# Kernel tuning notes

Hardware: AMD Instinct MI355X
Metric: run time of the kernel (lower is better)

The kernel has to match this reference:

```python
import jax, jax.numpy as jnp
import numpy as np

B, T, C, NH, RD = 128, 512, 384, 6, 16
HD = C // NH
SEQ_LEN = 512


def setup_inputs() -> dict:
    key = jax.random.key(0)
    kx, kqkv, kout = jax.random.split(key, 3)
    x = jax.random.normal(kx, (B, T, C), dtype=jnp.float32)
    # torch nn.Linear weights are [out_features, in_features]
    Wqkv = jax.random.normal(kqkv, (3 * C, C), dtype=jnp.float32) * 0.02
    Wout = jax.random.normal(kout, (C, C), dtype=jnp.float32) * 0.02
    freqs = 1.0 / (10000.0 ** (jnp.arange(0, RD, 2, dtype=jnp.float32) / RD))  # [RD//2]
    f = jnp.outer(jnp.arange(SEQ_LEN, dtype=jnp.float32), freqs)  # [SEQ_LEN, RD//2]
    cos = jnp.cos(f)[None, None]  # [1,1,SEQ_LEN,RD//2]
    sin = jnp.sin(f)[None, None]
    return {"x": x, "Wqkv": Wqkv, "Wout": Wout, "cos": cos, "sin": sin}


def _rope(t, c, s, rd):
    # t: [B, NH, T, HD]; partial rotary on first rd channels
    r, p = t[..., :rd], t[..., rd:]
    r1, r2 = r[..., : rd // 2], r[..., rd // 2:]
    rot = jnp.concatenate([r1 * c - r2 * s, r2 * c + r1 * s], axis=-1)
    return jnp.concatenate([rot, p], axis=-1)


def reference(x, Wqkv, Wout, cos, sin):
    b, t, c = x.shape
    nh, hd, rd = NH, c // NH, RD
    qkv = jnp.einsum("btc,dc->btd", x, Wqkv).reshape(b, t, 3, nh, hd)
    q, k, v = (jnp.transpose(qkv[:, :, i], (0, 2, 1, 3)) for i in range(3))  # [b,nh,t,hd]
    cc = cos[:, :, :t]
    ss = sin[:, :, :t]
    q = _rope(q, cc, ss, rd)
    k = _rope(k, cc, ss, rd)
    scale = 1.0 / jnp.sqrt(jnp.asarray(hd, dtype=x.dtype))
    scores = jnp.einsum("bhqd,bhkd->bhqk", q, k) * scale
    causal = jnp.tril(jnp.ones((t, t), dtype=bool))
    scores = jnp.where(causal, scores, jnp.finfo(scores.dtype).min)
    att = jax.nn.softmax(scores, axis=-1)
    o = jnp.einsum("bhqk,bhkd->bhqd", att, v)  # [b,nh,t,hd]
    o = jnp.transpose(o, (0, 2, 1, 3)).reshape(b, t, c)
    return jnp.einsum("btc,dc->btd", o, Wout)
```

## Files before the change

kernel.cpp:

```cpp
#include <hip/hip_runtime.h>

#define B_DIM 128
#define T_DIM 512
#define C_DIM 384
#define NH_DIM 6
#define HD_DIM 64
#define QKV_LD 1152

typedef __bf16 bf16x8 __attribute__((ext_vector_type(8)));
typedef __bf16 bf16x4 __attribute__((ext_vector_type(4)));
typedef float f32x4 __attribute__((ext_vector_type(4)));

#define K_SCALE 0.18033688011112042f

__device__ __forceinline__ void gload_lds16(const __bf16* g, __bf16* l) {
  __builtin_amdgcn_global_load_lds(
      (const __attribute__((address_space(1))) void*)g,
      (__attribute__((address_space(3))) void*)l, 16, 0, 0);
}

#define X_F4 6291456
#define WQKV_F4 110592
#define WOUT_F4 36864
__global__ __launch_bounds__(256) void cast_all(const float* __restrict__ x,
                                                const float* __restrict__ wqkv,
                                                const float* __restrict__ wout,
                                                __bf16* __restrict__ xb,
                                                __bf16* __restrict__ wqkvb,
                                                __bf16* __restrict__ woutb) {
  int i = blockIdx.x * blockDim.x + threadIdx.x;
  const float4* src;
  bf16x4* dst;
  if (i < X_F4) {
    src = (const float4*)x + i;
    dst = (bf16x4*)xb + i;
  } else if (i < X_F4 + WQKV_F4) {
    src = (const float4*)wqkv + (i - X_F4);
    dst = (bf16x4*)wqkvb + (i - X_F4);
  } else {
    src = (const float4*)wout + (i - X_F4 - WQKV_F4);
    dst = (bf16x4*)woutb + (i - X_F4 - WQKV_F4);
  }
  float4 v = *src;
  bf16x4 o;
  o[0] = (__bf16)v.x; o[1] = (__bf16)v.y; o[2] = (__bf16)v.z; o[3] = (__bf16)v.w;
  *dst = o;
}

__global__ __launch_bounds__(256) void gemm_bt(const __bf16* __restrict__ A,
                                               const __bf16* __restrict__ Bm,
                                               __bf16* __restrict__ Cbq,
                                               __bf16* __restrict__ Cbk,
                                               __bf16* __restrict__ vt,
                                               float* __restrict__ Cf,
                                               const float* __restrict__ cosp,
                                               const float* __restrict__ sinp,
                                               int M, int N, int K) {
  __shared__ __attribute__((aligned(16))) __bf16 As[128 * 32];
  __shared__ __attribute__((aligned(16))) __bf16 Bs[128 * 32];
  const int nwg = gridDim.x * gridDim.y;
  const int bid = blockIdx.x + gridDim.x * blockIdx.y;
  const int per = nwg >> 3;
  const int swz = (bid & 7) * per + (bid >> 3);
  const int m0 = (swz / gridDim.x) * 128;
  const int n0 = (swz % gridDim.x) * 128;
  const int tid = threadIdx.x;
  const int wave = tid >> 6;
  const int lane = tid & 63;
  const int lr = lane & 15;
  const int quad = lane >> 4;
  const int wm = (wave & 1) * 64;
  const int wn = (wave >> 1) * 64;
  const int ca0 = wave * 2, ca1 = wave * 2 + 1;
  const int srow = lane >> 2;
  const int row0 = ca0 * 16 + srow, row1 = ca1 * 16 + srow;
  const int slot = (lane & 3) ^ ((lane >> 3) & 3);
  const int rs = (quad ^ ((lr >> 1) & 3)) * 8;
  const __bf16* pA0 = &A[(size_t)(m0 + row0) * K + slot * 8];
  const __bf16* pA1 = &A[(size_t)(m0 + row1) * K + slot * 8];
  const __bf16* pB0 = &Bm[(size_t)(n0 + row0) * K + slot * 8];
  const __bf16* pB1 = &Bm[(size_t)(n0 + row1) * K + slot * 8];
  f32x4 acc[4][4] = {};
  for (int k0 = 0; k0 < K; k0 += 32) {
    __syncthreads();
    gload_lds16(pA0, &As[ca0 * 512]);
    gload_lds16(pA1, &As[ca1 * 512]);
    gload_lds16(pB0, &Bs[ca0 * 512]);
    gload_lds16(pB1, &Bs[ca1 * 512]);
    pA0 += 32; pA1 += 32; pB0 += 32; pB1 += 32;
    __syncthreads();
    bf16x8 af[4], bf[4];
#pragma unroll
    for (int i = 0; i < 4; ++i)
      af[i] = *(bf16x8*)&As[(wm + i * 16 + lr) * 32 + rs];
#pragma unroll
    for (int j = 0; j < 4; ++j)
      bf[j] = *(bf16x8*)&Bs[(wn + j * 16 + lr) * 32 + rs];
#pragma unroll
    for (int i = 0; i < 4; ++i)
#pragma unroll
      for (int j = 0; j < 4; ++j)
        acc[i][j] = __builtin_amdgcn_mfma_f32_16x16x32_bf16(af[i], bf[j], acc[i][j], 0, 0, 0);
  }
  if (Cf) {
#pragma unroll
    for (int i = 0; i < 4; ++i)
#pragma unroll
      for (int j = 0; j < 4; ++j) {
        int gm = m0 + wm + i * 16 + quad * 4;
        int gn = n0 + wn + j * 16 + lr;
#pragma unroll
        for (int r = 0; r < 4; ++r) Cf[(size_t)(gm + r) * N + gn] = acc[i][j][r];
      }
    return;
  }
  if (n0 >= 2 * C_DIM) {
    const int tbase = (m0 & (T_DIM - 1)) + wm;
    const int bb = m0 >> 9;
    const int dcolbase = n0 - 2 * C_DIM + wn;
    const int tslotx = (lane & 7) ^ (lane >> 3);
#pragma unroll
    for (int pass = 0; pass < 2; ++pass) {
      __syncthreads();
      if ((wave >> 1) == pass) {
        __bf16* T = (wave & 1) ? Bs : As;
#pragma unroll
        for (int i = 0; i < 4; ++i)
#pragma unroll
          for (int j = 0; j < 4; ++j) {
            const int d = j * 16 + lr;
            const int sl = (i * 2 + (quad >> 1)) ^ (d & 7);
            bf16x4 w;
#pragma unroll
            for (int r = 0; r < 4; ++r) w[r] = (__bf16)acc[i][j][r];
            *(bf16x4*)&T[d * 64 + sl * 8 + (quad & 1) * 4] = w;
          }
#pragma unroll
        for (int it = 0; it < 8; ++it) {
          const int dl = it * 8 + (lane >> 3);
          bf16x8 v = *(bf16x8*)&T[dl * 64 + (lane & 7) * 8];
          const int dfull = dcolbase + dl;
          const int hh = dfull >> 6, dd = dfull & 63;
          *(bf16x8*)&vt[((size_t)(bb * NH_DIM + hh) * 64 + dd) * T_DIM + tbase +
                        tslotx * 8] = v;
        }
      }
    }
    return;
  }
  const bool isQ = (n0 < C_DIM);
  __bf16* dst = isQ ? Cbq : Cbk;
  const int colbase = n0 - (isQ ? 0 : C_DIM);
  const float qs = isQ ? K_SCALE : 1.0f;
#pragma unroll
  for (int i = 0; i < 4; ++i) {
#pragma unroll
    for (int j = 0; j < 4; ++j) {
      int gm = m0 + wm + i * 16 + quad * 4;
      int gn = colbase + wn + j * 16 + lr;
      const int cbase = colbase + wn + j * 16;
      const bool ropeBlk = ((cbase & 63) == 0);
      if (ropeBlk) {
#pragma unroll
        for (int r = 0; r < 4; ++r) {
          float v = acc[i][j][r];
          float p = __shfl_xor(v, 8, 64);
          int t = (gm + r) & (T_DIM - 1);
          float c = cosp[t * 8 + (lr & 7)];
          float s = sinp[t * 8 + (lr & 7)];
          v = (lr & 8) ? __builtin_fmaf(v, c, p * s)
                       : __builtin_fmaf(v, c, -p * s);
          dst[(size_t)(gm + r) * C_DIM + gn] = (__bf16)(v * qs);
        }
      } else {
#pragma unroll
        for (int r = 0; r < 4; ++r)
          dst[(size_t)(gm + r) * C_DIM + gn] = (__bf16)(acc[i][j][r] * qs);
      }
    }
  }
}

__global__ __launch_bounds__(256) void attn_kernel(const __bf16* __restrict__ qb,
                                                   const __bf16* __restrict__ kb,
                                                   const __bf16* __restrict__ vt,
                                                   __bf16* __restrict__ o) {
  __shared__ __attribute__((aligned(16))) __bf16 K0s[64 * 64];
  __shared__ __attribute__((aligned(16))) __bf16 K1s[64 * 64];
  __shared__ __attribute__((aligned(16))) __bf16 V0s[64 * 64];
  __shared__ __attribute__((aligned(16))) __bf16 V1s[64 * 64];
  const int bid = blockIdx.x;
  const int swz = (bid & 7) * 384 + (bid >> 3);
  const int pair = swz & 3;
  const int h = (swz >> 2) % NH_DIM;
  const int b = swz / (4 * NH_DIM);
  const int qlo = pair, qhi = 7 - pair;
  const int tid = threadIdx.x;
  const int wave = tid >> 6;
  const int lane = tid & 63;
  const int lr = lane & 15;
  const int quad = lane >> 4;
  const __bf16* qbase = qb + (size_t)b * T_DIM * C_DIM + h * HD_DIM;
  const __bf16* kbase = kb + (size_t)b * T_DIM * C_DIM + h * HD_DIM;
  const __bf16* vtb = vt + (size_t)(b * NH_DIM + h) * HD_DIM * T_DIM;
  const int qrow_lo = qlo * 64 + wave * 16;
  const int qrow_hi = qhi * 64 + wave * 16;
  bf16x8 qfl[2], qfh[2];
#pragma unroll
  for (int ks = 0; ks < 2; ++ks) {
    qfl[ks] = *(const bf16x8*)&qbase[(size_t)(qrow_lo + lr) * C_DIM + ks * 32 + quad * 8];
    qfh[ks] = *(const bf16x8*)&qbase[(size_t)(qrow_hi + lr) * C_DIM + ks * 32 + quad * 8];
  }
  f32x4 oaL[4] = {}, oaH[4] = {};
  f32x4 lL = {}, lH = {};
  bf16x8 vones;
#pragma unroll
  for (int e = 0; e < 8; ++e) vones[e] = (__bf16)1.0f;
  const int skey = (((lane >> 3) & 3) << 1) | (wave & 1);
  const int gsl = ((lane & 7) ^ skey) * 8;
  const int grA = wave * 8 + (lane >> 3);
  const int grB = grA + 32;
  const int ldsA = wave * 512;
  const int ldsB = (wave + 4) * 512;
  auto stage = [&](int kt, __bf16* KT, __bf16* VT) {
    const __bf16* ks = kbase + (size_t)(kt * 64) * C_DIM;
    const __bf16* vs = vtb + kt * 64;
    gload_lds16(&ks[(size_t)grA * C_DIM + gsl], KT + ldsA);
    gload_lds16(&ks[(size_t)grB * C_DIM + gsl], KT + ldsB);
    gload_lds16(&vs[(size_t)grA * T_DIM + gsl], VT + ldsA);
    gload_lds16(&vs[(size_t)grB * T_DIM + gsl], VT + ldsB);
  };
  const int keyK = ((lr & 3) << 1) | ((lr >> 2) & 1);
  const int keyV = ((lr & 3) << 1) | ((lr >> 3) & 1);
  const int swK0 = (quad ^ keyK) * 8, swK1 = ((4 + quad) ^ keyK) * 8;
  const int swV0 = (quad ^ keyV) * 8, swV1 = ((4 + quad) ^ keyV) * 8;
  const int rkbase = ((lr >> 2) & 3) * 8 + (lr & 3);
  auto body = [&](const __bf16* KT, const __bf16* VT, const bf16x8 (&qf)[2],
                  f32x4 (&oa)[4], f32x4& lacc, int myq, bool diag, int kt) {
    f32x4 sj[4];
#pragma unroll
    for (int j = 0; j < 4; ++j) {
      const int rK = (j >> 1) * 32 + (j & 1) * 4 + rkbase;
      bf16x8 kf0 = *(const bf16x8*)&KT[rK * 64 + swK0];
      bf16x8 kf1 = *(const bf16x8*)&KT[rK * 64 + swK1];
      f32x4 z = {};
      z = __builtin_amdgcn_mfma_f32_16x16x32_bf16(kf0, qf[0], z, 0, 0, 0);
      z = __builtin_amdgcn_mfma_f32_16x16x32_bf16(kf1, qf[1], z, 0, 0, 0);
      sj[j] = z;
    }
    if (diag) {
#pragma unroll
      for (int j = 0; j < 4; ++j)
#pragma unroll
        for (int r = 0; r < 4; ++r) {
          int key = kt * 64 + (j >> 1) * 32 + quad * 8 + (j & 1) * 4 + r;
          if (key > myq) sj[j][r] = -3.0e38f;
        }
    }
    bf16x8 pf0, pf1;
#pragma unroll
    for (int j = 0; j < 4; ++j)
#pragma unroll
      for (int r = 0; r < 4; ++r) {
        float pv = exp2f(sj[j][r]);
        const int jj = (j & 1) * 4 + r;
        if (j < 2) pf0[jj] = (__bf16)pv; else pf1[jj] = (__bf16)pv;
      }
#pragma unroll
    for (int dt = 0; dt < 4; ++dt) {
      bf16x8 vf0 = *(const bf16x8*)&VT[(dt * 16 + lr) * 64 + swV0];
      bf16x8 vf1 = *(const bf16x8*)&VT[(dt * 16 + lr) * 64 + swV1];
      oa[dt] = __builtin_amdgcn_mfma_f32_16x16x32_bf16(pf0, vf0, oa[dt], 0, 0, 0);
      oa[dt] = __builtin_amdgcn_mfma_f32_16x16x32_bf16(pf1, vf1, oa[dt], 0, 0, 0);
    }
    lacc = __builtin_amdgcn_mfma_f32_16x16x32_bf16(pf0, vones, lacc, 0, 0, 0);
    lacc = __builtin_amdgcn_mfma_f32_16x16x32_bf16(pf1, vones, lacc, 0, 0, 0);
  };
  stage(0, K0s, V0s);
  __syncthreads();
  int kt = 0;
  while (true) {
    if (kt < qhi) stage(kt + 1, K1s, V1s);
    if (kt <= qlo) body(K0s, V0s, qfl, oaL, lL, qrow_lo + lr, kt == qlo, kt);
    body(K0s, V0s, qfh, oaH, lH, qrow_hi + lr, kt == qhi, kt);
    __syncthreads();
    ++kt;
    if (kt > qhi) break;
    if (kt < qhi) stage(kt + 1, K0s, V0s);
    if (kt <= qlo) body(K1s, V1s, qfl, oaL, lL, qrow_lo + lr, kt == qlo, kt);
    body(K1s, V1s, qfh, oaH, lH, qrow_hi + lr, kt == qhi, kt);
    __syncthreads();
    ++kt;
    if (kt > qhi) break;
  }
#pragma unroll
  for (int r = 0; r < 4; ++r) {
    float ilL = 1.0f / lL[r];
    float ilH = 1.0f / lH[r];
#pragma unroll
    for (int dt = 0; dt < 4; ++dt) {
      size_t rowL = (size_t)b * T_DIM + qrow_lo + quad * 4 + r;
      size_t rowH = (size_t)b * T_DIM + qrow_hi + quad * 4 + r;
      o[rowL * C_DIM + h * HD_DIM + dt * 16 + lr] = (__bf16)(oaL[dt][r] * ilL);
      o[rowH * C_DIM + h * HD_DIM + dt * 16 + lr] = (__bf16)(oaH[dt][r] * ilH);
    }
  }
}

extern "C" void kernel_launch(void* const* d_in, const int* in_sizes, int n_in,
                              void* d_out, int out_size, void* d_ws, size_t ws_size,
                              hipStream_t stream) {
  const float* x    = (const float*)d_in[0];
  const float* wqkv = (const float*)d_in[1];
  const float* wout = (const float*)d_in[2];
  const float* cosp = (const float*)d_in[3];
  const float* sinp = (const float*)d_in[4];
  float* out = (float*)d_out;

  char* ws = (char*)d_ws;
  __bf16* xb    = (__bf16*)(ws);
  __bf16* qb    = (__bf16*)(ws + 50331648);
  __bf16* kb    = (__bf16*)(ws + 100663296);
  __bf16* vtb   = (__bf16*)(ws + 150994944);
  __bf16* ob    = (__bf16*)(ws + 201326592);
  __bf16* wqkvb = (__bf16*)(ws + 251658240);
  __bf16* woutb = (__bf16*)(ws + 252542976);

  const int M = B_DIM * T_DIM;

  cast_all<<<25152, 256, 0, stream>>>(x, wqkv, wout, xb, wqkvb, woutb);

  gemm_bt<<<dim3(QKV_LD / 128, M / 128), 256, 0, stream>>>(
      xb, wqkvb, qb, kb, vtb, (float*)nullptr, cosp, sinp, M, QKV_LD, C_DIM);

  attn_kernel<<<3072, 256, 0, stream>>>(qb, kb, vtb, ob);

  gemm_bt<<<dim3(C_DIM / 128, M / 128), 256, 0, stream>>>(
      ob, woutb, (__bf16*)nullptr, (__bf16*)nullptr, (__bf16*)nullptr, out,
      (const float*)nullptr, (const float*)nullptr, M, C_DIM, C_DIM);
}
```

Before: 372.5 us.

## Swap MFMA operand order to transpose accumulators and vectorize epilogue stores

```diff
diff --git a/kernel.cpp b/kernel.cpp
--- a/kernel.cpp
+++ b/kernel.cpp
@@ -100,49 +100,34 @@
     for (int i = 0; i < 4; ++i)
 #pragma unroll
       for (int j = 0; j < 4; ++j)
-        acc[i][j] = __builtin_amdgcn_mfma_f32_16x16x32_bf16(af[i], bf[j], acc[i][j], 0, 0, 0);
+        acc[i][j] = __builtin_amdgcn_mfma_f32_16x16x32_bf16(bf[j], af[i], acc[i][j], 0, 0, 0);
   }
   if (Cf) {
 #pragma unroll
-    for (int i = 0; i < 4; ++i)
+    for (int i = 0; i < 4; ++i) {
+      const int gm = m0 + wm + i * 16 + lr;
 #pragma unroll
       for (int j = 0; j < 4; ++j) {
-        int gm = m0 + wm + i * 16 + quad * 4;
-        int gn = n0 + wn + j * 16 + lr;
-#pragma unroll
-        for (int r = 0; r < 4; ++r) Cf[(size_t)(gm + r) * N + gn] = acc[i][j][r];
+        const int gn = n0 + wn + j * 16 + quad * 4;
+        *(f32x4*)&Cf[(size_t)gm * N + gn] = acc[i][j];
       }
+    }
     return;
   }
   if (n0 >= 2 * C_DIM) {
-    const int tbase = (m0 & (T_DIM - 1)) + wm;
+    const int tb = (m0 & (T_DIM - 1)) + wm;
     const int bb = m0 >> 9;
-    const int dcolbase = n0 - 2 * C_DIM + wn;
-    const int tslotx = (lane & 7) ^ (lane >> 3);
-#pragma unroll
-    for (int pass = 0; pass < 2; ++pass) {
-      __syncthreads();
-      if ((wave >> 1) == pass) {
-        __bf16* T = (wave & 1) ? Bs : As;
-#pragma unroll
-        for (int i = 0; i < 4; ++i)
-#pragma unroll
-          for (int j = 0; j < 4; ++j) {
-            const int d = j * 16 + lr;
-            const int sl = (i * 2 + (quad >> 1)) ^ (d & 7);
-            bf16x4 w;
-#pragma unroll
-            for (int r = 0; r < 4; ++r) w[r] = (__bf16)acc[i][j][r];
-            *(bf16x4*)&T[d * 64 + sl * 8 + (quad & 1) * 4] = w;
-          }
-#pragma unroll
-        for (int it = 0; it < 8; ++it) {
-          const int dl = it * 8 + (lane >> 3);
-          bf16x8 v = *(bf16x8*)&T[dl * 64 + (lane & 7) * 8];
-          const int dfull = dcolbase + dl;
+    const int dcb = n0 - 2 * C_DIM + wn;
+#pragma unroll
+    for (int i = 0; i < 4; ++i) {
+      const int t = tb + i * 16 + lr;
+#pragma unroll
+      for (int j = 0; j < 4; ++j) {
+#pragma unroll
+        for (int r = 0; r < 4; ++r) {
+          const int dfull = dcb + j * 16 + quad * 4 + r;
           const int hh = dfull >> 6, dd = dfull & 63;
-          *(bf16x8*)&vt[((size_t)(bb * NH_DIM + hh) * 64 + dd) * T_DIM + tbase +
-                        tslotx * 8] = v;
+          vt[((size_t)(bb * NH_DIM + hh) * 64 + dd) * T_DIM + t] = (__bf16)acc[i][j][r];
         }
       }
     }
@@ -150,33 +135,32 @@
   }
   const bool isQ = (n0 < C_DIM);
   __bf16* dst = isQ ? Cbq : Cbk;
-  const int colbase = n0 - (isQ ? 0 : C_DIM);
+  const int colb0 = n0 - (isQ ? 0 : C_DIM);
   const float qs = isQ ? K_SCALE : 1.0f;
 #pragma unroll
   for (int i = 0; i < 4; ++i) {
+    const int gm = m0 + wm + i * 16 + lr;
+    const int t = gm & (T_DIM - 1);
 #pragma unroll
     for (int j = 0; j < 4; ++j) {
-      int gm = m0 + wm + i * 16 + quad * 4;
-      int gn = colbase + wn + j * 16 + lr;
-      const int cbase = colbase + wn + j * 16;
-      const bool ropeBlk = ((cbase & 63) == 0);
-      if (ropeBlk) {
+      const int cb = colb0 + wn + j * 16;
+      bf16x4 w;
+      if ((cb & 63) == 0) {
 #pragma unroll
         for (int r = 0; r < 4; ++r) {
           float v = acc[i][j][r];
-          float p = __shfl_xor(v, 8, 64);
-          int t = (gm + r) & (T_DIM - 1);
-          float c = cosp[t * 8 + (lr & 7)];
-          float s = sinp[t * 8 + (lr & 7)];
-          v = (lr & 8) ? __builtin_fmaf(v, c, p * s)
-                       : __builtin_fmaf(v, c, -p * s);
-          dst[(size_t)(gm + r) * C_DIM + gn] = (__bf16)(v * qs);
+          float p = __shfl_xor(v, 32, 64);
+          float c = cosp[t * 8 + (quad & 1) * 4 + r];
+          float s = sinp[t * 8 + (quad & 1) * 4 + r];
+          v = (quad & 2) ? __builtin_fmaf(v, c, p * s)
+                         : __builtin_fmaf(v, c, -p * s);
+          w[r] = (__bf16)(v * qs);
         }
       } else {
 #pragma unroll
-        for (int r = 0; r < 4; ++r)
-          dst[(size_t)(gm + r) * C_DIM + gn] = (__bf16)(acc[i][j][r] * qs);
+        for (int r = 0; r < 4; ++r) w[r] = (__bf16)(acc[i][j][r] * qs);
       }
+      *(bf16x4*)&dst[(size_t)gm * C_DIM + cb + quad * 4] = w;
     }
   }
 }
@@ -270,11 +254,11 @@
     for (int dt = 0; dt < 4; ++dt) {
       bf16x8 vf0 = *(const bf16x8*)&VT[(dt * 16 + lr) * 64 + swV0];
       bf16x8 vf1 = *(const bf16x8*)&VT[(dt * 16 + lr) * 64 + swV1];
-      oa[dt] = __builtin_amdgcn_mfma_f32_16x16x32_bf16(pf0, vf0, oa[dt], 0, 0, 0);
-      oa[dt] = __builtin_amdgcn_mfma_f32_16x16x32_bf16(pf1, vf1, oa[dt], 0, 0, 0);
-    }
-    lacc = __builtin_amdgcn_mfma_f32_16x16x32_bf16(pf0, vones, lacc, 0, 0, 0);
-    lacc = __builtin_amdgcn_mfma_f32_16x16x32_bf16(pf1, vones, lacc, 0, 0, 0);
+      oa[dt] = __builtin_amdgcn_mfma_f32_16x16x32_bf16(vf0, pf0, oa[dt], 0, 0, 0);
+      oa[dt] = __builtin_amdgcn_mfma_f32_16x16x32_bf16(vf1, pf1, oa[dt], 0, 0, 0);
+    }
+    lacc = __builtin_amdgcn_mfma_f32_16x16x32_bf16(vones, pf0, lacc, 0, 0, 0);
+    lacc = __builtin_amdgcn_mfma_f32_16x16x32_bf16(vones, pf1, lacc, 0, 0, 0);
   };
   stage(0, K0s, V0s);
   __syncthreads();
@@ -293,17 +277,21 @@
     ++kt;
     if (kt > qhi) break;
   }
-#pragma unroll
-  for (int r = 0; r < 4; ++r) {
-    float ilL = 1.0f / lL[r];
-    float ilH = 1.0f / lH[r];
-#pragma unroll
-    for (int dt = 0; dt < 4; ++dt) {
-      size_t rowL = (size_t)b * T_DIM + qrow_lo + quad * 4 + r;
-      size_t rowH = (size_t)b * T_DIM + qrow_hi + quad * 4 + r;
-      o[rowL * C_DIM + h * HD_DIM + dt * 16 + lr] = (__bf16)(oaL[dt][r] * ilL);
-      o[rowH * C_DIM + h * HD_DIM + dt * 16 + lr] = (__bf16)(oaH[dt][r] * ilH);
-    }
+  const float ilL = 1.0f / lL[0];
+  const float ilH = 1.0f / lH[0];
+  const size_t rowL = (size_t)b * T_DIM + qrow_lo + lr;
+  const size_t rowH = (size_t)b * T_DIM + qrow_hi + lr;
+#pragma unroll
+  for (int dt = 0; dt < 4; ++dt) {
+    bf16x4 wL, wH;
+#pragma unroll
+    for (int r = 0; r < 4; ++r) {
+      wL[r] = (__bf16)(oaL[dt][r] * ilL);
+      wH[r] = (__bf16)(oaH[dt][r] * ilH);
+    }
+    const int col = h * HD_DIM + dt * 16 + quad * 4;
+    *(bf16x4*)&o[rowL * C_DIM + col] = wL;
+    *(bf16x4*)&o[rowH * C_DIM + col] = wH;
   }
 }
 
```

Result: slower. 408.2 us (+9.6%).
